# Performance work log

Measured on AMD Instinct MI355X. Metric: run time of the kernel, lower is better.

The kernel has to match this reference:

```python
import jax, jax.numpy as jnp
import numpy as np

B, C, L = 8, 512, 2048   # batch, input_dim (channels), sequence length
H = 8                    # multihead_cnt
K = 3                    # kernel_dim
DH = C // H              # per-head dim = 64
SCALE = 1.0 / float(np.sqrt(C))  # module divides by sqrt(input_dim), not sqrt(head_dim)


def _conv1d(x, w, b):
    # x: [B, C, L], w: [C_out, C_in, K], padding=1 keeps L
    y = jax.lax.conv_general_dilated(x, w, window_strides=(1,), padding=[(1, 1)],
                                     dimension_numbers=('NCH', 'OIH', 'NCH'))
    return y + b[None, :, None]


def setup_inputs() -> dict:
    key = jax.random.key(0)
    ks = jax.random.split(key, 7)
    x = jax.random.normal(ks[0], (B, C, L), dtype=jnp.float32)
    # xavier_normal_ std for Conv1d weight [C, C, K]: sqrt(2 / (fan_in + fan_out)), fan = C*K
    std = float(np.sqrt(2.0 / (C * K + C * K)))
    inp = {'x': x}
    for i in range(3):  # conv_cnt = 3 -> q, k, v convolutions
        inp[f'w{i}'] = jax.random.normal(ks[1 + 2 * i], (C, C, K), dtype=jnp.float32) * std
        inp[f'b{i}'] = jax.random.normal(ks[2 + 2 * i], (C,), dtype=jnp.float32) * 0.01
    return inp


def reference(x, w0, b0, w1, b1, w2, b2):
    # q, k, v projections via Conv1d (padding preserves length)
    q = _conv1d(x, w0, b0)  # [B, C, L]
    k = _conv1d(x, w1, b1)
    v = _conv1d(x, w2, b2)
    # torch.chunk along dim 1 == contiguous reshape into heads
    qh = q.reshape(B, H, DH, L)
    kh = k.reshape(B, H, DH, L)
    vh = v.reshape(B, H, DH, L)
    # scores = q^T k / sqrt(input_dim)  -> [B, H, L, L]
    scores = jnp.einsum('bhdl,bhdm->bhlm', qh, kh) * SCALE
    att = jax.nn.softmax(scores, axis=-1)
    # out = (att @ v^T)^T -> [B, H, DH, L]
    out = jnp.einsum('bhlm,bhdm->bhdl', att, vh)
    return out.reshape(B, C, L)
```

## Files before the change

### kernel.cpp

```cpp
#include <hip/hip_runtime.h>
#include <hip/hip_bf16.h>
#include <cstdint>

typedef unsigned short u16;
typedef short v8s __attribute__((ext_vector_type(8)));
typedef float v4f __attribute__((ext_vector_type(4)));
typedef u16 u16x8 __attribute__((ext_vector_type(8)));
typedef u16 u16x4 __attribute__((ext_vector_type(4)));

static constexpr int Bb = 8, Cc = 512, Ll = 2048, Hh = 8, Dh = 64;

__device__ __forceinline__ float bf2f(u16 u){
  unsigned x = ((unsigned)u) << 16; float f; __builtin_memcpy(&f, &x, 4); return f;
}
__device__ __forceinline__ u16 f2bf(float f){
  unsigned x; __builtin_memcpy(&x, &f, 4);
  x = (x + 0x7fffu + ((x >> 16) & 1u)) >> 16; return (u16)x;
}

__device__ __forceinline__ void async_cp16(const u16* g, u16* l){
  __builtin_amdgcn_global_load_lds(
      (const __attribute__((address_space(1))) unsigned int*)g,
      (__attribute__((address_space(3))) unsigned int*)l, 16, 0, 0);
}

#if __has_builtin(__builtin_amdgcn_exp2f)
#define EXP2F(x) __builtin_amdgcn_exp2f(x)
#else
#define EXP2F(x) exp2f(x)
#endif

__global__ __launch_bounds__(256) void detect_dtype(const u16* __restrict__ x, unsigned* __restrict__ flag){
  __shared__ int cnt;
  if (threadIdx.x == 0) cnt = 0;
  __syncthreads();
  int sane = 0;
  for (int i = threadIdx.x; i < 4096; i += 256){
    unsigned e = (x[2 * i] >> 7) & 0xFFu;
    sane += (e >= 90u && e <= 160u) ? 1 : 0;
  }
  atomicAdd(&cnt, sane);
  __syncthreads();
  if (threadIdx.x == 0) *flag = (cnt < 2458) ? 1u : 0u;
}

__global__ __launch_bounds__(256) void transpose_pad(const void* __restrict__ xv, const unsigned* __restrict__ flagp,
                                                     u16* __restrict__ xT){
  int b = blockIdx.z, ci0 = blockIdx.y * 64, l0 = blockIdx.x * 64;
  __shared__ u16 tb[64 * 72];
  const unsigned isf32 = *flagp;
  int t = threadIdx.x;
  int row = t >> 3, seg = t & 7;
  if (isf32){
    const float* xf = (const float*)xv;
    #pragma unroll
    for (int rnd = 0; rnd < 2; rnd++){
      int ci = row + rnd * 32;
      size_t off = ((size_t)(b * Cc + ci0 + ci)) * Ll + l0 + seg * 8;
      v4f a = *(const v4f*)(xf + off);
      v4f c4 = *(const v4f*)(xf + off + 4);
      #pragma unroll
      for (int j = 0; j < 4; j++) tb[(seg * 8 + j) * 72 + ci] = f2bf(a[j]);
      #pragma unroll
      for (int j = 0; j < 4; j++) tb[(seg * 8 + 4 + j) * 72 + ci] = f2bf(c4[j]);
    }
  } else {
    const u16* x = (const u16*)xv;
    #pragma unroll
    for (int rnd = 0; rnd < 2; rnd++){
      int ci = row + rnd * 32;
      u16x8 v = *(const u16x8*)(x + ((size_t)(b * Cc + ci0 + ci)) * Ll + l0 + seg * 8);
      #pragma unroll
      for (int j = 0; j < 8; j++) tb[(seg * 8 + j) * 72 + ci] = v[j];
    }
  }
  __syncthreads();
  #pragma unroll
  for (int rnd = 0; rnd < 2; rnd++){
    int l = row + rnd * 32;
    u16x8 v = *(const u16x8*)&tb[l * 72 + seg * 8];
    *(u16x8*)(xT + ((size_t)b * 2050 + 1 + l0 + l) * Cc + ci0 + seg * 8) = v;
  }
  if (blockIdx.x == 0 && t < 8){
    u16x8 z = {};
    *(u16x8*)(xT + ((size_t)b * 2050 + 0) * Cc + ci0 + t * 8) = z;
  }
  if (blockIdx.x == 31 && t < 8){
    u16x8 z = {};
    *(u16x8*)(xT + ((size_t)b * 2050 + 2049) * Cc + ci0 + t * 8) = z;
  }
}

__global__ __launch_bounds__(256) void pack_wb(const void* __restrict__ w0, const void* __restrict__ w1,
                                               const void* __restrict__ w2, const void* __restrict__ b0,
                                               const void* __restrict__ b1, const void* __restrict__ b2,
                                               const unsigned* __restrict__ flagp,
                                               u16* __restrict__ wp, u16* __restrict__ bb){
  int g = blockIdx.x * 256 + threadIdx.x;
  const unsigned isf32 = *flagp;
  if (g < 9 * 512 * 512){
    int ci = g & 511, co = (g >> 9) & 511, kc = g >> 18;
    int conv = kc / 3, k = kc - conv * 3;
    const void* w = (conv == 0) ? w0 : ((conv == 1) ? w1 : w2);
    size_t idx = (size_t)co * 1536 + ci * 3 + k;
    wp[g] = isf32 ? f2bf(((const float*)w)[idx]) : ((const u16*)w)[idx];
  } else {
    int g2 = g - 9 * 512 * 512;
    if (g2 < 1536){
      int conv = g2 >> 9, c = g2 & 511;
      const void* bsrc = (conv == 0) ? b0 : ((conv == 1) ? b1 : b2);
      bb[g2] = isf32 ? f2bf(((const float*)bsrc)[c]) : ((const u16*)bsrc)[c];
    }
  }
}

__global__ __launch_bounds__(512, 2) void conv_gemm_fused(const u16* __restrict__ wp, const u16* __restrict__ xT,
                                                          const u16* __restrict__ bb, u16* __restrict__ qT,
                                                          u16* __restrict__ kT, u16* __restrict__ vN){
  __shared__ u16 smem[49152];
  int bx = blockIdx.x;
  int b = bx & 7, inner = bx >> 3;
  int mt = inner >> 3, nt = inner & 7;
  int m0 = mt << 7, n0 = nt << 8;
  int conv = m0 >> 9, co0 = m0 & 511;

  int t = threadIdx.x, wave = t >> 6, lane = t & 63, quad = lane >> 4, lid = lane & 15;
  int wm_i = wave >> 2, wn_i = wave & 3;

  int sx = (lid & 7) << 4;
  int cb0 = ((quad * 16) ^ sx) >> 1;
  int cb1 = ((64 + quad * 16) ^ sx) >> 1;
  int abase0 = (wm_i * 64 + lid) * 64;
  int bbase0 = 8192 + (wn_i * 64 + lid) * 64;

  int srcA[2], srcB[4];
  #pragma unroll
  for (int r = 0; r < 2; r++){
    int p = t * 16 + r * 8192;
    int row = p >> 7, c = (p & 127) ^ ((row & 7) << 4);
    srcA[r] = row * 512 + (c >> 1);
  }
  #pragma unroll
  for (int r = 0; r < 4; r++){
    int p = t * 16 + r * 8192;
    int row = p >> 7, c = (p & 127) ^ ((row & 7) << 4);
    srcB[r] = row * 512 + (c >> 1);
  }
  int dA0 = t * 8, dA1 = t * 8 + 4096;

  const u16* aGbase = wp + (size_t)(conv * 1536 + co0) * 512;
  const u16* bGbase = xT + (size_t)b * (2050 * 512) + (size_t)n0 * 512;

#define STAGE_TILE(aG, bG, stg) do{ \
    async_cp16((aG) + srcA[0], (stg) + dA0); \
    async_cp16((aG) + srcA[1], (stg) + dA1); \
    _Pragma("unroll") for (int r = 0; r < 4; ++r) \
      async_cp16((bG) + srcB[r], (stg) + 8192 + t * 8 + r * 4096); }while(0)

#define LOAD_A() do{ \
    _Pragma("unroll") for (int m = 0; m < 4; ++m){ \
      af[m][0] = *(const v8s*)(lds + abase0 + m * 1024 + cb0); \
      af[m][1] = *(const v8s*)(lds + abase0 + m * 1024 + cb1); } }while(0)

#define LOAD_Bn(n) do{ \
    bfc[0] = *(const v8s*)(lds + bbase0 + (n) * 1024 + cb0); \
    bfc[1] = *(const v8s*)(lds + bbase0 + (n) * 1024 + cb1); }while(0)

#define MFMA_COL(n) do{ \
    __builtin_amdgcn_s_setprio(1); \
    _Pragma("unroll") for (int m = 0; m < 4; ++m) \
    _Pragma("unroll") for (int kh = 0; kh < 2; ++kh) \
      acc[m][n] = __builtin_amdgcn_mfma_f32_16x16x32_bf16(af[m][kh], bfc[kh], acc[m][n], 0, 0, 0); \
    __builtin_amdgcn_s_setprio(0); }while(0)

  v4f acc[4][4] = {};
  v8s af[4][2], bfc[2];

  STAGE_TILE(aGbase, bGbase, smem);
  asm volatile("s_waitcnt vmcnt(0)" ::: "memory");
  __builtin_amdgcn_sched_barrier(0);
  __builtin_amdgcn_s_barrier();

  #pragma unroll 2
  for (int kt = 0; kt < 24; ++kt){
    u16* lds = smem + (kt & 1) * 24576;
    u16* stg = smem + ((kt + 1) & 1) * 24576;
    if (kt < 23){
      int k1 = kt + 1;
      int ks1 = k1 >> 3, ci1 = (k1 & 7) << 6;
      const u16* aG = aGbase + (size_t)ks1 * 262144 + ci1;
      const u16* bG = bGbase + (size_t)ks1 * 512 + ci1;
      STAGE_TILE(aG, bG, stg);
    }
    LOAD_A();
    LOAD_Bn(0); MFMA_COL(0);
    LOAD_Bn(1); MFMA_COL(1);
    LOAD_Bn(2); MFMA_COL(2);
    LOAD_Bn(3); MFMA_COL(3);
    if (kt < 23){
      asm volatile("s_waitcnt vmcnt(0)" ::: "memory");
      __builtin_amdgcn_sched_barrier(0);
      __builtin_amdgcn_s_barrier();
    }
  }

#undef STAGE_TILE
#undef LOAD_A
#undef LOAD_Bn
#undef MFMA_COL

  const float qsc = (float)(1.4426950408889634 / 22.627416997969522);
  if (conv < 2){
    u16* dst = (conv == 0) ? qT : kT;
    #pragma unroll
    for (int m = 0; m < 4; ++m){
      int cog = m0 + wm_i * 64 + m * 16 + quad * 4;
      float bv[4];
      #pragma unroll
      for (int r = 0; r < 4; r++) bv[r] = bf2f(bb[cog + r]);
      int coc = cog & 511;
      #pragma unroll
      for (int n = 0; n < 4; ++n){
        int l = n0 + wn_i * 64 + n * 16 + lid;
        u16x4 pk;
        #pragma unroll
        for (int r = 0; r < 4; r++){
          float v = acc[m][n][r] + bv[r];
          if (conv == 0) v *= qsc;
          pk[r] = f2bf(v);
        }
        *(u16x4*)(dst + ((((size_t)b * Hh + (coc >> 6)) * Ll + l) << 6) + (coc & 63)) = pk;
      }
    }
  } else {
    u16* scr = smem;
    __syncthreads();
    #pragma unroll
    for (int m = 0; m < 4; ++m){
      int rloc = wm_i * 64 + m * 16 + quad * 4;
      int cog = m0 + rloc;
      float bv[4];
      #pragma unroll
      for (int r = 0; r < 4; r++) bv[r] = bf2f(bb[cog + r]);
      #pragma unroll
      for (int n = 0; n < 4; ++n){
        int lcl = wn_i * 64 + n * 16 + lid;
        #pragma unroll
        for (int r = 0; r < 4; r++)
          scr[(rloc + r) * 264 + lcl] = f2bf(acc[m][n][r] + bv[r]);
      }
    }
    __syncthreads();
    int seg = t & 31, rw = t >> 5;
    #pragma unroll
    for (int ps = 0; ps < 8; ++ps){
      int row = rw + ps * 16;
      u16x8 vv = *(const u16x8*)&scr[row * 264 + seg * 8];
      *(u16x8*)(vN + (((size_t)b * Cc + co0 + row) << 11) + n0 + seg * 8) = vv;
    }
  }
}

__global__ __launch_bounds__(256) void attn_kernel(const u16* __restrict__ qT, const u16* __restrict__ kT,
                                                   const u16* __restrict__ vN, const unsigned* __restrict__ flagp,
                                                   void* __restrict__ outv){
  int bhx = blockIdx.x;
  int b = bhx >> 3, h = bhx & 7, l0 = blockIdx.y * 128;
  int t = threadIdx.x, w = t >> 6, lane = t & 63, quad = lane >> 4, lid = lane & 15;
  __shared__ u16 kls[128 * 72];
  __shared__ u16 vls[64 * 136];
  const unsigned isf32 = *flagp;
  const size_t bh = (size_t)b * Hh + h;

  int kadd[5], vadd[5];
  bool kval[5], vval[5];
  #pragma unroll
  for (int r = 0; r < 5; r++){
    int e = (r * 256 + t) * 8;
    kval[r] = e < 128 * 72;
    int slot = e / 72, off = e - slot * 72;
    int s5 = slot & 31;
    int m = (slot & ~31) | (((s5 >> 2) & 1) << 3) | (((s5 >> 3) & 1) << 4) | (((s5 >> 4) & 1) << 2) | (s5 & 3);
    kadd[r] = m * 64 + (off < 64 ? off : 0);
    vval[r] = e < 64 * 136;
    int d = e / 136, voff = e - d * 136;
    vadd[r] = d * Ll + (voff < 128 ? voff : 0);
  }
  const u16* kTb = kT + bh * Ll * 64;
  const u16* vNb = vN + ((size_t)(b * Cc + h * Dh)) * Ll;

  v8s qF[2][2];
  #pragma unroll
  for (int ci = 0; ci < 2; ci++)
    #pragma unroll
    for (int ks = 0; ks < 2; ks++)
      qF[ci][ks] = *(const v8s*)(qT + ((bh * Ll) + l0 + w * 32 + ci * 16 + lid) * 64 + ks * 32 + quad * 8);

  const v8s onesF = {0x3F80, 0x3F80, 0x3F80, 0x3F80, 0x3F80, 0x3F80, 0x3F80, 0x3F80};
  v4f o[2][4] = {};
  v4f o1[2] = {};

  for (int mt = 0; mt < 16; mt++){
    int m0 = mt * 128;
    const u16* kt = kTb + (size_t)m0 * 64;
    const u16* vt = vNb + m0;
    #pragma unroll
    for (int r = 0; r < 5; r++)
      if (kval[r]) async_cp16(kt + kadd[r], &kls[(r * 256 + t) * 8]);
    #pragma unroll
    for (int r = 0; r < 5; r++)
      if (vval[r]) async_cp16(vt + vadd[r], &vls[(r * 256 + t) * 8]);
    __syncthreads();

    v4f s[4][2][2] = {};
    #pragma unroll
    for (int ks = 0; ks < 2; ks++){
      v8s aF[4][2];
      #pragma unroll
      for (int c = 0; c < 4; c++)
        #pragma unroll
        for (int tt = 0; tt < 2; tt++)
          aF[c][tt] = *(const v8s*)&kls[(c * 32 + tt * 16 + lid) * 72 + ks * 32 + quad * 8];
      #pragma unroll
      for (int c = 0; c < 4; c++)
        #pragma unroll
        for (int tt = 0; tt < 2; tt++){
          s[c][tt][0] = __builtin_amdgcn_mfma_f32_16x16x32_bf16(aF[c][tt], qF[0][ks], s[c][tt][0], 0, 0, 0);
          s[c][tt][1] = __builtin_amdgcn_mfma_f32_16x16x32_bf16(aF[c][tt], qF[1][ks], s[c][tt][1], 0, 0, 0);
        }
    }

    #pragma unroll
    for (int c = 0; c < 4; c++){
      v8s aP[2];
      #pragma unroll
      for (int ci = 0; ci < 2; ci++){
        float p[8];
        #pragma unroll
        for (int tt = 0; tt < 2; tt++)
          #pragma unroll
          for (int r = 0; r < 4; r++)
            p[tt * 4 + r] = EXP2F(s[c][tt][ci][r]);
        unsigned u[4];
        #pragma unroll
        for (int k2 = 0; k2 < 4; k2++){
          __hip_bfloat162 hb = __float22bfloat162_rn(make_float2(p[2 * k2], p[2 * k2 + 1]));
          __builtin_memcpy(&u[k2], &hb, 4);
        }
        __builtin_memcpy(&aP[ci], u, 16);
      }
      v8s bV[4];
      #pragma unroll
      for (int df = 0; df < 4; df++)
        bV[df] = *(const v8s*)&vls[(df * 16 + lid) * 136 + c * 32 + quad * 8];
      #pragma unroll
      for (int ci = 0; ci < 2; ci++){
        #pragma unroll
        for (int df = 0; df < 4; df++)
          o[ci][df] = __builtin_amdgcn_mfma_f32_16x16x32_bf16(aP[ci], bV[df], o[ci][df], 0, 0, 0);
        o1[ci] = __builtin_amdgcn_mfma_f32_16x16x32_bf16(aP[ci], onesF, o1[ci], 0, 0, 0);
      }
    }
    __syncthreads();
  }

  #pragma unroll
  for (int lf = 0; lf < 2; lf++){
    v4f nv;
    #pragma unroll
    for (int r = 0; r < 4; r++) nv[r] = 1.f / o1[lf][r];
    #pragma unroll
    for (int df = 0; df < 4; df++){
      int d = df * 16 + lid;
      int l = l0 + w * 32 + lf * 16 + quad * 4;
      size_t ofs = (((bh << 6) + d) << 11) + l;
      if (isf32){
        v4f st;
        #pragma unroll
        for (int r = 0; r < 4; r++) st[r] = o[lf][df][r] * nv[r];
        *(v4f*)((float*)outv + ofs) = st;
      } else {
        u16x4 pk;
        #pragma unroll
        for (int r = 0; r < 4; r++) pk[r] = f2bf(o[lf][df][r] * nv[r]);
        *(u16x4*)((u16*)outv + ofs) = pk;
      }
    }
  }
}

extern "C" void kernel_launch(void* const* d_in, const int* in_sizes, int n_in,
                              void* d_out, int out_size, void* d_ws, size_t ws_size,
                              hipStream_t stream){
  const void* x  = d_in[0];
  const void* w0 = d_in[1];
  const void* b0 = d_in[2];
  const void* w1 = d_in[3];
  const void* b1 = d_in[4];
  const void* w2 = d_in[5];
  const void* b2 = d_in[6];
  u16* ws = (u16*)d_ws;
  unsigned* flag = (unsigned*)ws;
  u16* xT = ws + 64;
  u16* wp = xT + (size_t)8 * 2050 * 512;
  u16* bb = wp + (size_t)9 * 512 * 512;
  u16* qT = bb + 1536;
  u16* kT = qT + (size_t)8 * 8 * 2048 * 64;
  u16* vN = kT + (size_t)8 * 8 * 2048 * 64;

  detect_dtype<<<1, 256, 0, stream>>>((const u16*)x, flag);
  transpose_pad<<<dim3(32, 8, 8), 256, 0, stream>>>(x, flag, xT);
  pack_wb<<<dim3(9 * 512 * 512 / 256 + 6), 256, 0, stream>>>(w0, w1, w2, b0, b1, b2, flag, wp, bb);
  conv_gemm_fused<<<dim3(768), 512, 0, stream>>>(wp, xT, bb, qT, kT, vN);
  attn_kernel<<<dim3(64, 16), 256, 0, stream>>>(qT, kT, vN, flag, d_out);
}
```

Baseline: 270.3 us.

## Triple-buffer conv GEMM and double-buffer K/V with XOR-swizzled LDS in attention

The conv GEMM moves from double to triple buffering in LDS, prefetching two k-steps ahead and using partial vmcnt waits so global loads overlap more compute. The attention kernel double-buffers its K and V tiles, prefetching the next tile while computing the current one. It also replaces padded LDS rows with XOR-swizzled addressing and splits the waits so QK^T can start before V has landed. This adds LDS usage, which may reduce occupancy, and relies on hand-counted vmcnt values being correct.

```diff
diff --git a/kernel.cpp b/kernel.cpp
--- a/kernel.cpp
+++ b/kernel.cpp
@@ -117,7 +117,7 @@
 __global__ __launch_bounds__(512, 2) void conv_gemm_fused(const u16* __restrict__ wp, const u16* __restrict__ xT,
                                                           const u16* __restrict__ bb, u16* __restrict__ qT,
                                                           u16* __restrict__ kT, u16* __restrict__ vN){
-  __shared__ u16 smem[49152];
+  __shared__ u16 smem[73728];
   int bx = blockIdx.x;
   int b = bx & 7, inner = bx >> 3;
   int mt = inner >> 3, nt = inner & 7;
@@ -177,19 +177,20 @@
   v8s af[4][2], bfc[2];
 
   STAGE_TILE(aGbase, bGbase, smem);
-  asm volatile("s_waitcnt vmcnt(0)" ::: "memory");
+  STAGE_TILE(aGbase + 64, bGbase + 64, smem + 24576);
+  asm volatile("s_waitcnt vmcnt(6)" ::: "memory");
   __builtin_amdgcn_sched_barrier(0);
   __builtin_amdgcn_s_barrier();
 
-  #pragma unroll 2
+  #pragma unroll 3
   for (int kt = 0; kt < 24; ++kt){
-    u16* lds = smem + (kt & 1) * 24576;
-    u16* stg = smem + ((kt + 1) & 1) * 24576;
-    if (kt < 23){
-      int k1 = kt + 1;
-      int ks1 = k1 >> 3, ci1 = (k1 & 7) << 6;
-      const u16* aG = aGbase + (size_t)ks1 * 262144 + ci1;
-      const u16* bG = bGbase + (size_t)ks1 * 512 + ci1;
+    u16* lds = smem + (kt % 3) * 24576;
+    if (kt < 22){
+      int k2 = kt + 2;
+      int ks2 = k2 >> 3, ci2 = (k2 & 7) << 6;
+      const u16* aG = aGbase + (size_t)ks2 * 262144 + ci2;
+      const u16* bG = bGbase + (size_t)ks2 * 512 + ci2;
+      u16* stg = smem + (k2 % 3) * 24576;
       STAGE_TILE(aG, bG, stg);
     }
     LOAD_A();
@@ -197,7 +198,11 @@
     LOAD_Bn(1); MFMA_COL(1);
     LOAD_Bn(2); MFMA_COL(2);
     LOAD_Bn(3); MFMA_COL(3);
-    if (kt < 23){
+    if (kt < 22){
+      asm volatile("s_waitcnt vmcnt(6)" ::: "memory");
+      __builtin_amdgcn_sched_barrier(0);
+      __builtin_amdgcn_s_barrier();
+    } else if (kt == 22){
       asm volatile("s_waitcnt vmcnt(0)" ::: "memory");
       __builtin_amdgcn_sched_barrier(0);
       __builtin_amdgcn_s_barrier();
@@ -267,27 +272,33 @@
   int bhx = blockIdx.x;
   int b = bhx >> 3, h = bhx & 7, l0 = blockIdx.y * 128;
   int t = threadIdx.x, w = t >> 6, lane = t & 63, quad = lane >> 4, lid = lane & 15;
-  __shared__ u16 kls[128 * 72];
-  __shared__ u16 vls[64 * 136];
+  __shared__ u16 kls[2][128 * 64];
+  __shared__ u16 vls[2][64 * 128];
   const unsigned isf32 = *flagp;
   const size_t bh = (size_t)b * Hh + h;
-
-  int kadd[5], vadd[5];
-  bool kval[5], vval[5];
-  #pragma unroll
-  for (int r = 0; r < 5; r++){
+  const int xk = (lid & 7) << 3;
+
+  int kadd[4], vadd[4];
+  #pragma unroll
+  for (int r = 0; r < 4; r++){
     int e = (r * 256 + t) * 8;
-    kval[r] = e < 128 * 72;
-    int slot = e / 72, off = e - slot * 72;
+    int slot = e >> 6, col = e & 63;
     int s5 = slot & 31;
     int m = (slot & ~31) | (((s5 >> 2) & 1) << 3) | (((s5 >> 3) & 1) << 4) | (((s5 >> 4) & 1) << 2) | (s5 & 3);
-    kadd[r] = m * 64 + (off < 64 ? off : 0);
-    vval[r] = e < 64 * 136;
-    int d = e / 136, voff = e - d * 136;
-    vadd[r] = d * Ll + (voff < 128 ? voff : 0);
+    kadd[r] = m * 64 + (col ^ ((slot & 7) << 3));
+    int d = e >> 7, m8 = e & 127;
+    vadd[r] = d * Ll + (m8 ^ ((d & 7) << 3));
   }
   const u16* kTb = kT + bh * Ll * 64;
   const u16* vNb = vN + ((size_t)(b * Cc + h * Dh)) * Ll;
+
+#define STAGE_KV(mt1) do{ \
+    const u16* kp = kTb + (size_t)(mt1) * 8192; \
+    const u16* vp = vNb + (mt1) * 128; \
+    u16* kd = &kls[(mt1) & 1][0]; \
+    u16* vd = &vls[(mt1) & 1][0]; \
+    _Pragma("unroll") for (int r = 0; r < 4; r++) async_cp16(kp + kadd[r], kd + (r * 256 + t) * 8); \
+    _Pragma("unroll") for (int r = 0; r < 4; r++) async_cp16(vp + vadd[r], vd + (r * 256 + t) * 8); }while(0)
 
   v8s qF[2][2];
   #pragma unroll
@@ -300,17 +311,15 @@
   v4f o[2][4] = {};
   v4f o1[2] = {};
 
+  STAGE_KV(0);
+  asm volatile("s_waitcnt vmcnt(4)" ::: "memory");
+  __builtin_amdgcn_sched_barrier(0);
+  __builtin_amdgcn_s_barrier();
+
   for (int mt = 0; mt < 16; mt++){
-    int m0 = mt * 128;
-    const u16* kt = kTb + (size_t)m0 * 64;
-    const u16* vt = vNb + m0;
-    #pragma unroll
-    for (int r = 0; r < 5; r++)
-      if (kval[r]) async_cp16(kt + kadd[r], &kls[(r * 256 + t) * 8]);
-    #pragma unroll
-    for (int r = 0; r < 5; r++)
-      if (vval[r]) async_cp16(vt + vadd[r], &vls[(r * 256 + t) * 8]);
-    __syncthreads();
+    if (mt < 15) STAGE_KV(mt + 1);
+    const u16* kcur = &kls[mt & 1][0];
+    const u16* vcur = &vls[mt & 1][0];
 
     v4f s[4][2][2] = {};
     #pragma unroll
@@ -320,7 +329,8 @@
       for (int c = 0; c < 4; c++)
         #pragma unroll
         for (int tt = 0; tt < 2; tt++)
-          aF[c][tt] = *(const v8s*)&kls[(c * 32 + tt * 16 + lid) * 72 + ks * 32 + quad * 8];
+          aF[c][tt] = *(const v8s*)&kcur[(c * 32 + tt * 16 + lid) * 64 + ((ks * 32 + quad * 8) ^ xk)];
+      __builtin_amdgcn_s_setprio(1);
       #pragma unroll
       for (int c = 0; c < 4; c++)
         #pragma unroll
@@ -328,7 +338,16 @@
           s[c][tt][0] = __builtin_amdgcn_mfma_f32_16x16x32_bf16(aF[c][tt], qF[0][ks], s[c][tt][0], 0, 0, 0);
           s[c][tt][1] = __builtin_amdgcn_mfma_f32_16x16x32_bf16(aF[c][tt], qF[1][ks], s[c][tt][1], 0, 0, 0);
         }
-    }
+      __builtin_amdgcn_s_setprio(0);
+    }
+
+    if (mt < 15){
+      asm volatile("s_waitcnt vmcnt(8)" ::: "memory");
+    } else {
+      asm volatile("s_waitcnt vmcnt(0)" ::: "memory");
+    }
+    __builtin_amdgcn_sched_barrier(0);
+    __builtin_amdgcn_s_barrier();
 
     #pragma unroll
     for (int c = 0; c < 4; c++){
@@ -352,7 +371,8 @@
       v8s bV[4];
       #pragma unroll
       for (int df = 0; df < 4; df++)
-        bV[df] = *(const v8s*)&vls[(df * 16 + lid) * 136 + c * 32 + quad * 8];
+        bV[df] = *(const v8s*)&vcur[(df * 16 + lid) * 128 + ((c * 32 + quad * 8) ^ xk)];
+      __builtin_amdgcn_s_setprio(1);
       #pragma unroll
       for (int ci = 0; ci < 2; ci++){
         #pragma unroll
@@ -360,9 +380,16 @@
           o[ci][df] = __builtin_amdgcn_mfma_f32_16x16x32_bf16(aP[ci], bV[df], o[ci][df], 0, 0, 0);
         o1[ci] = __builtin_amdgcn_mfma_f32_16x16x32_bf16(aP[ci], onesF, o1[ci], 0, 0, 0);
       }
-    }
-    __syncthreads();
-  }
+      __builtin_amdgcn_s_setprio(0);
+    }
+
+    if (mt < 15){
+      asm volatile("s_waitcnt vmcnt(4)" ::: "memory");
+      __builtin_amdgcn_sched_barrier(0);
+      __builtin_amdgcn_s_barrier();
+    }
+  }
+#undef STAGE_KV
 
   #pragma unroll
   for (int lf = 0; lf < 2; lf++){
```

New measurement: 263.1 us. -2.7%, faster.
